# Optimization experiments

Measured on AMD Instinct MI355X. Metric: run time of the kernel, lower is better.

## Reference

```python
import jax, jax.numpy as jnp
import numpy as np

# (pt, eta, phi) feature indices per particle for each block (eta=None for MET)
A_PT, A_ETA, A_PHI = [5, 4, 35, 34], [9, 8, 45, 44], [13, 12, 55, 54]            # e3,e2,j9,j8
B_PT, B_ETA, B_PHI = [3, 33, 31, 2], [7, 43, 41, 6], [11, 53, 51, 10]            # e1,j7,j5,e0
C_PT, C_ETA, C_PHI = [28, 32, 15, 16], [38, 42, 19, 20], [48, 52, 23, 24]        # j2,j6,mu1,mu2
D_PT, D_ETA, D_PHI = [0, 14, 30, 26, 29, 27, 17], [None, 18, 40, 36, 39, 37, 21], [1, 22, 50, 46, 49, 47, 25]  # MET,mu0,j4,j0,j3,j1,mu3


def _bc(a, nd):
    # broadcast a (B,) or () angle factor over nd trailing qubit axes
    return a.reshape(a.shape + (1,) * nd)


def _rx(state, theta, w):
    nd = state.ndim - 2
    c = _bc(jnp.cos(theta * 0.5), nd)
    s = _bc(jnp.sin(theta * 0.5), nd)
    s0 = jnp.take(state, 0, axis=w + 1)
    s1 = jnp.take(state, 1, axis=w + 1)
    return jnp.stack([c * s0 - 1j * s * s1, -1j * s * s0 + c * s1], axis=w + 1)


def _ry(state, theta, w):
    nd = state.ndim - 2
    c = _bc(jnp.cos(theta * 0.5), nd)
    s = _bc(jnp.sin(theta * 0.5), nd)
    s0 = jnp.take(state, 0, axis=w + 1)
    s1 = jnp.take(state, 1, axis=w + 1)
    return jnp.stack([c * s0 - s * s1, s * s0 + c * s1], axis=w + 1)


def _rz(state, theta, w):
    nd = state.ndim - 2
    ph = _bc(jnp.exp(-0.5j * theta.astype(state.dtype)), nd)
    s0 = jnp.take(state, 0, axis=w + 1)
    s1 = jnp.take(state, 1, axis=w + 1)
    return jnp.stack([ph * s0, jnp.conj(ph) * s1], axis=w + 1)


def _cnot(state, ctrl, tgt):
    c0 = jnp.take(state, 0, axis=ctrl + 1)
    c1 = jnp.take(state, 1, axis=ctrl + 1)
    t_ax = tgt + 1 if tgt < ctrl else tgt  # ctrl axis removed shifts higher wires down
    c1 = jnp.flip(c1, axis=t_ax)
    return jnp.stack([c0, c1], axis=ctrl + 1)


def _extract(x, pt_idx, eta_idx, phi_idx):
    pt = x[:, np.array(pt_idx)]
    eta = jnp.stack([x[:, i] if i is not None else jnp.zeros(x.shape[0], x.dtype) for i in eta_idx], axis=1)
    phi = x[:, np.array(phi_idx)]
    return pt, eta, phi


def _run_block(pt, eta, phi, weights, n, latent, trash, depth):
    B = pt.shape[0]
    state = jnp.zeros((B,) + (2,) * n, dtype=jnp.complex64)
    state = state.at[(slice(None),) + (0,) * n].set(1.0)
    for k in range(n):
        state = _rx(state, eta[:, k], k)
        state = _ry(state, pt[:, k], k)
        state = _rz(state, phi[:, k], k)
    for k in range(n - 1):
        state = _cnot(state, k, k + 1)
    for k in range(n):
        state = _rz(state, eta[:, k], k)
        state = _ry(state, pt[:, k], k)
        state = _rx(state, phi[:, k], k)
    for d in range(depth):
        for t in trash:
            for l in latent:
                state = _cnot(state, t, l)
        for k in range(n):
            state = _ry(state, weights[d * n + k], k)
        for l in latent:
            for t in trash:
                state = _cnot(state, l, t)
    p = jnp.abs(state) ** 2  # (B, 2,...,2) real probabilities
    red = tuple(range(1, n))
    zs = [jnp.sum(jnp.take(p, 0, axis=w + 1), axis=red) - jnp.sum(jnp.take(p, 1, axis=w + 1), axis=red) for w in trash]
    return jnp.stack(zs, axis=1)


def setup_inputs() -> dict:
    key = jax.random.key(0)
    k0, k1, k2, k3, k4 = jax.random.split(key, 5)
    B = 131072
    x = jax.random.normal(k0, (B, 56), dtype=jnp.float32)
    wA = 0.01 * jax.random.normal(k1, (4,), dtype=jnp.float32)
    wB = 0.01 * jax.random.normal(k2, (4,), dtype=jnp.float32)
    wC = 0.01 * jax.random.normal(k3, (4,), dtype=jnp.float32)
    wD = 0.01 * jax.random.normal(k4, (28,), dtype=jnp.float32)
    return {"x": x, "wA": wA, "wB": wB, "wC": wC, "wD": wD}


def reference(x, wA, wB, wC, wD):
    zA = _run_block(*_extract(x, A_PT, A_ETA, A_PHI), wA, 4, (0, 1), (2, 3), 1)  # (B,2)
    zB = _run_block(*_extract(x, B_PT, B_ETA, B_PHI), wB, 4, (0, 1), (2, 3), 1)  # (B,2)
    zC = _run_block(*_extract(x, C_PT, C_ETA, C_PHI), wC, 4, (0, 1), (2, 3), 1)  # (B,2)
    zD = _run_block(*_extract(x, D_PT, D_ETA, D_PHI), wD, 7, (0, 1, 2, 3), (4, 5, 6), 4)  # (B,3)
    return jnp.concatenate([zA, zB, zC, zD], axis=1)  # (B,9) ~ dict values concatenated
```

## Files before the change

kernel.cpp:

```cpp
#include <hip/hip_runtime.h>
#include <hip/hip_fp16.h>


#define DEVINL __device__ __forceinline__

typedef _Float16 hv2 __attribute__((ext_vector_type(2)));

struct C2 { __half2 rr, mp; };

DEVINL C2 mkc(float re, float im) {
  C2 c; c.rr = __floats2half2_rn(re, re); c.mp = __floats2half2_rn(-im, im); return c;
}
DEVINL __half2 mkamp(float re, float im) { return __floats2half2_rn(re, im); }
DEVINL __half2 swap2(__half2 v) { return __lowhigh2highlow(v); }
DEVINL __half2 cmulc(C2 u, __half2 v) { return __hfma2(u.rr, v, __hmul2(u.mp, swap2(v))); }

DEVINL float ampsq(__half2 v, float acc) {
#if __has_builtin(__builtin_amdgcn_fdot2)
  return __builtin_amdgcn_fdot2(__builtin_bit_cast(hv2, v), __builtin_bit_cast(hv2, v), acc, false);
#else
  float2 f = __half22float2(v);
  return fmaf(f.x, f.x, fmaf(f.y, f.y, acc));
#endif
}

constexpr int parc(int x) { x ^= x >> 4; x ^= x >> 2; x ^= x >> 1; return x & 1; }

struct c32 { float x, y; };
DEVINL c32 cmulf(c32 a, c32 b) { return { a.x*b.x - a.y*b.y, a.x*b.y + a.y*b.x }; }


template<int N, int W>
DEVINL void g_ry(__half2* a, __half2 c2, __half2 s2, __half2 ns2) {
  constexpr int M = 1 << (N - 1 - W);
#pragma unroll
  for (int i = 0; i < (1 << N); ++i) if (!(i & M)) {
    const int j = i | M;
    __half2 v0 = a[i], v1 = a[j];
    a[i] = __hfma2(c2, v0, __hmul2(ns2, v1));
    a[j] = __hfma2(c2, v1, __hmul2(s2, v0));
  }
}

template<int N, int W>
DEVINL void g_u2(__half2* a, C2 u00, C2 u01, C2 u10, C2 u11) {
  constexpr int M = 1 << (N - 1 - W);
#pragma unroll
  for (int i = 0; i < (1 << N); ++i) if (!(i & M)) {
    const int j = i | M;
    __half2 v0 = a[i], v1 = a[j], v0s = swap2(v0), v1s = swap2(v1);
    a[i] = __hfma2(u00.rr, v0, __hfma2(u00.mp, v0s, __hfma2(u01.rr, v1, __hmul2(u01.mp, v1s))));
    a[j] = __hfma2(u10.rr, v0, __hfma2(u10.mp, v0s, __hfma2(u11.rr, v1, __hmul2(u11.mp, v1s))));
  }
}

template<int N, int C, int T>
DEVINL void g_cnot(__half2* a) {
  constexpr int CM = 1 << (N - 1 - C), TM = 1 << (N - 1 - T);
#pragma unroll
  for (int i = 0; i < (1 << N); ++i) if ((i & CM) && !(i & TM)) {
    const int j = i | TM;
    __half2 t = a[i]; a[i] = a[j]; a[j] = t;
  }
}

template<int N, int K>
DEVINL void chain_cnot(__half2* a) {
  if constexpr (K < N - 1) { g_cnot<N, K, K + 1>(a); chain_cnot<N, K + 1>(a); }
}


DEVINL void mk_u01(float ce, float se, float cp, float sp, float cf, float sf,
                   c32& u0, c32& u1) {
  u0 = cmulf({cf, -sf}, {cp * ce, sp * se});
  u1 = cmulf({cf,  sf}, {sp * ce, -cp * se});
}

DEVINL void mk_U(float ce, float se, float cp, float sp, float cf, float sf,
                 C2& U00, C2& U01, C2& U10, C2& U11) {
  c32 z = {ce, -se}, zb = {ce, se};
  c32 A = cmulf({cf * cp, -sf * sp}, z);
  c32 T = cmulf({cf * sp,  sf * cp}, zb);
  c32 Cc = cmulf({cf * sp, -sf * cp}, z);
  c32 D = cmulf({cf * cp,  sf * sp}, zb);
  U00 = mkc(A.x, A.y); U01 = mkc(-T.x, -T.y); U10 = mkc(Cc.x, Cc.y); U11 = mkc(D.x, D.y);
}

template<int N, int M>
DEVINL void build_step(__half2* a, const float* ce, const float* se, const float* cp,
                       const float* sp, const float* cf, const float* sf) {
  if constexpr (M < N) {
    c32 u0, u1; mk_u01(ce[M], se[M], cp[M], sp[M], cf[M], sf[M], u0, u1);
    C2 c0 = mkc(u0.x, u0.y), c1 = mkc(u1.x, u1.y);
#pragma unroll
    for (int j = (1 << M) - 1; j >= 0; --j) {
      __half2 s = a[j];
      a[2 * j]     = cmulc(c0, s);
      a[2 * j + 1] = cmulc(c1, s);
    }
    build_step<N, M + 1>(a, ce, se, cp, sp, cf, sf);
  }
}

template<int N, int K>
DEVINL void u_sweep(__half2* a, const float* ce, const float* se, const float* cp,
                    const float* sp, const float* cf, const float* sf) {
  if constexpr (K < N) {
    C2 U00, U01, U10, U11;
    mk_U(ce[K], se[K], cp[K], sp[K], cf[K], sf[K], U00, U01, U10, U11);
    g_u2<N, K>(a, U00, U01, U10, U11);
    u_sweep<N, K + 1>(a, ce, se, cp, sp, cf, sf);
  }
}

template<int N, int K>
DEVINL void ry_sweep(__half2* a, const __half2* c2, const __half2* s2, const __half2* ns2) {
  if constexpr (K < N) {
    g_ry<N, K>(a, c2[K], s2[K], ns2[K]);
    ry_sweep<N, K + 1>(a, c2, s2, ns2);
  }
}


template<int I>
DEVINL void sim4h(const float* r, const float* __restrict__ w, float* z) {
  constexpr int PT[3][4]  = {{5, 4, 35, 34}, {3, 33, 31, 2}, {28, 32, 15, 16}};
  constexpr int ETA[3][4] = {{9, 8, 45, 44}, {7, 43, 41, 6}, {38, 42, 19, 20}};
  constexpr int PHI[3][4] = {{13, 12, 55, 54}, {11, 53, 51, 10}, {48, 52, 23, 24}};
  float ce[4], se[4], cp[4], sp[4], cf[4], sf[4];
#pragma unroll
  for (int k = 0; k < 4; ++k) {
    __sincosf(0.5f * r[ETA[I][k]], &se[k], &ce[k]);
    __sincosf(0.5f * r[PT[I][k]],  &sp[k], &cp[k]);
    __sincosf(0.5f * r[PHI[I][k]], &sf[k], &cf[k]);
  }
  __half2 a[16];
  a[0] = mkamp(1.f, 0.f);
  build_step<4, 0>(a, ce, se, cp, sp, cf, sf);
  chain_cnot<4, 0>(a);
  u_sweep<4, 0>(a, ce, se, cp, sp, cf, sf);

#pragma unroll
  for (int i = 0; i < 16; ++i)
    if (parc(i & 3) && !(i & 8)) { __half2 t = a[i]; a[i] = a[i ^ 12]; a[i ^ 12] = t; }

  __half2 c2[4], s2[4], ns2[4];
#pragma unroll
  for (int k = 0; k < 4; ++k) {
    float sv, cv; __sincosf(0.5f * w[k], &sv, &cv);
    c2[k] = __floats2half2_rn(cv, cv);
    s2[k] = __floats2half2_rn(sv, sv);
    ns2[k] = __floats2half2_rn(-sv, -sv);
  }
  ry_sweep<4, 0>(a, c2, s2, ns2);

#pragma unroll
  for (int i = 0; i < 16; ++i)
    if (parc(i & 12) && !(i & 2)) { __half2 t = a[i]; a[i] = a[i ^ 3]; a[i ^ 3] = t; }

  float cls[4];
#pragma unroll
  for (int c = 0; c < 4; ++c) cls[c] = 0.f;
#pragma unroll
  for (int i = 0; i < 16; ++i) cls[i & 3] = ampsq(a[i], cls[i & 3]);
  float z0 = 0.f, z1 = 0.f;
#pragma unroll
  for (int c = 0; c < 4; ++c) {
    z0 += (c & 2) ? -cls[c] : cls[c];
    z1 += (c & 1) ? -cls[c] : cls[c];
  }
  z[0] = z0; z[1] = z1;
}


DEVINL void sim7h(const float* r, const float* __restrict__ wD, float* z) {
  constexpr int PT[7]  = {0, 14, 30, 26, 29, 27, 17};
  constexpr int ETA[7] = {-1, 18, 40, 36, 39, 37, 21};
  constexpr int PHI[7] = {1, 22, 50, 46, 49, 47, 25};
  float ce[7], se[7], cp[7], sp[7], cf[7], sf[7];
#pragma unroll
  for (int k = 0; k < 7; ++k) {
    float e = (ETA[k] < 0) ? 0.f : r[ETA[k]];
    __sincosf(0.5f * e, &se[k], &ce[k]);
    __sincosf(0.5f * r[PT[k]],  &sp[k], &cp[k]);
    __sincosf(0.5f * r[PHI[k]], &sf[k], &cf[k]);
  }
  __half2 a[128];
  a[0] = mkamp(1.f, 0.f);
  build_step<7, 0>(a, ce, se, cp, sp, cf, sf);
  chain_cnot<7, 0>(a);
  u_sweep<7, 0>(a, ce, se, cp, sp, cf, sf);

#pragma unroll 1
  for (int d = 0; d < 4; ++d) {
#pragma unroll
    for (int i = 0; i < 128; ++i)
      if (parc(i & 7) && !(i & 64)) { __half2 t = a[i]; a[i] = a[i ^ 0x78]; a[i ^ 0x78] = t; }

    __half2 c2[7], s2[7], ns2[7];
#pragma unroll
    for (int k = 0; k < 7; ++k) {
      float sv, cv; __sincosf(0.5f * wD[d * 7 + k], &sv, &cv);
      c2[k] = __floats2half2_rn(cv, cv);
      s2[k] = __floats2half2_rn(sv, sv);
      ns2[k] = __floats2half2_rn(-sv, -sv);
    }
    ry_sweep<7, 0>(a, c2, s2, ns2);

#pragma unroll
    for (int i = 0; i < 128; ++i)
      if (parc(i & 0x78) && !(i & 4)) { __half2 t = a[i]; a[i] = a[i ^ 7]; a[i ^ 7] = t; }
  }

  float cls[8];
#pragma unroll
  for (int c = 0; c < 8; ++c) cls[c] = 0.f;
#pragma unroll
  for (int i = 0; i < 128; ++i) cls[i & 7] = ampsq(a[i], cls[i & 7]);
  float z4 = 0.f, z5 = 0.f, z6 = 0.f;
#pragma unroll
  for (int c = 0; c < 8; ++c) {
    z4 += (c & 4) ? -cls[c] : cls[c];
    z5 += (c & 2) ? -cls[c] : cls[c];
    z6 += (c & 1) ? -cls[c] : cls[c];
  }
  z[0] = z4; z[1] = z5; z[2] = z6;
}


__global__ void __launch_bounds__(256, 2)
k_all(const float* __restrict__ x,
      const float* __restrict__ wA, const float* __restrict__ wB,
      const float* __restrict__ wC, const float* __restrict__ wD,
      float* __restrict__ out, int B) {
  const int b = blockIdx.x * blockDim.x + threadIdx.x;
  if (b >= B) return;

  float r[56];
  const float4* row4 = (const float4*)(x + (size_t)b * 56);
#pragma unroll
  for (int i = 0; i < 14; ++i) {
    float4 v = row4[i];
    r[4 * i] = v.x; r[4 * i + 1] = v.y; r[4 * i + 2] = v.z; r[4 * i + 3] = v.w;
  }

  float o[9];
  sim4h<0>(r, wA, &o[0]);
  sim4h<1>(r, wB, &o[2]);
  sim4h<2>(r, wC, &o[4]);
  sim7h(r, wD, &o[6]);

  float* op = out + (size_t)b * 9;
#pragma unroll
  for (int i = 0; i < 9; ++i) op[i] = o[i];
}


extern "C" void kernel_launch(void* const* d_in, const int* in_sizes, int n_in,
                              void* d_out, int out_size, void* d_ws, size_t ws_size,
                              hipStream_t stream) {
  const float* x  = (const float*)d_in[0];
  const float* wA = (const float*)d_in[1];
  const float* wB = (const float*)d_in[2];
  const float* wC = (const float*)d_in[3];
  const float* wD = (const float*)d_in[4];
  float* out = (float*)d_out;
  const int B = in_sizes[0] / 56;
  const int threads = 256;
  const int grid = (B + threads - 1) / threads;
  k_all<<<grid, threads, 0, stream>>>(x, wA, wB, wC, wD, out, B);
}
```

Measured before the change: 127.7 us.

## Split each event across two lanes with DPP exchange for the 7-qubit state

Each event is now handled by a pair of adjacent lanes. The lanes split blocks A and B between them, both compute block C redundantly, and the 7-qubit block D state is split by its top qubit into 64 amplitudes per lane. Gates on qubit 0 and the cross-half swaps use DPP lane exchanges, and the final Z sums are combined across the pair. The goal is to halve per-thread register pressure (128 to 64 half2 amplitudes) so occupancy can rise, with launch bounds raised to 3 blocks per SM. The cost is twice as many threads per event, redundant row loads and sincos work, and the duplicated block C computation.

```diff
diff --git a/kernel.cpp b/kernel.cpp
--- a/kernel.cpp
+++ b/kernel.cpp
@@ -24,6 +24,23 @@
 #endif
 }
 
+DEVINL __half2 dpph(__half2 v) {
+  int i = __builtin_bit_cast(int, v);
+  i = __builtin_amdgcn_mov_dpp(i, 0xB1, 0xF, 0xF, true);
+  return __builtin_bit_cast(__half2, i);
+}
+DEVINL float dppf(float v) {
+  int i = __builtin_bit_cast(int, v);
+  i = __builtin_amdgcn_mov_dpp(i, 0xB1, 0xF, 0xF, true);
+  return __builtin_bit_cast(float, i);
+}
+
+DEVINL __half2 selh(bool p, __half2 a, __half2 b) {
+  int ia = __builtin_bit_cast(int, a), ib = __builtin_bit_cast(int, b);
+  return __builtin_bit_cast(__half2, p ? ia : ib);
+}
+DEVINL float self_(bool p, float a, float b) { return p ? a : b; }
+
 constexpr int parc(int x) { x ^= x >> 4; x ^= x >> 2; x ^= x >> 1; return x & 1; }
 
 struct c32 { float x, y; };
@@ -64,11 +81,6 @@
   }
 }
 
-template<int N, int K>
-DEVINL void chain_cnot(__half2* a) {
-  if constexpr (K < N - 1) { g_cnot<N, K, K + 1>(a); chain_cnot<N, K + 1>(a); }
-}
-
 
 DEVINL void mk_u01(float ce, float se, float cp, float sp, float cf, float sf,
                    c32& u0, c32& u1) {
@@ -76,15 +88,23 @@
   u1 = cmulf({cf,  sf}, {sp * ce, -cp * se});
 }
 
+DEVINL void mk_Uf(float ce, float se, float cp, float sp, float cf, float sf,
+                  c32& A, c32& nT, c32& C, c32& D) {
+  c32 z = {ce, -se}, zb = {ce, se};
+  A = cmulf({cf * cp, -sf * sp}, z);
+  c32 T = cmulf({cf * sp,  sf * cp}, zb);
+  nT = {-T.x, -T.y};
+  C = cmulf({cf * sp, -sf * cp}, z);
+  D = cmulf({cf * cp,  sf * sp}, zb);
+}
+
 DEVINL void mk_U(float ce, float se, float cp, float sp, float cf, float sf,
                  C2& U00, C2& U01, C2& U10, C2& U11) {
-  c32 z = {ce, -se}, zb = {ce, se};
-  c32 A = cmulf({cf * cp, -sf * sp}, z);
-  c32 T = cmulf({cf * sp,  sf * cp}, zb);
-  c32 Cc = cmulf({cf * sp, -sf * cp}, z);
-  c32 D = cmulf({cf * cp,  sf * sp}, zb);
-  U00 = mkc(A.x, A.y); U01 = mkc(-T.x, -T.y); U10 = mkc(Cc.x, Cc.y); U11 = mkc(D.x, D.y);
-}
+  c32 A, nT, C, D;
+  mk_Uf(ce, se, cp, sp, cf, sf, A, nT, C, D);
+  U00 = mkc(A.x, A.y); U01 = mkc(nT.x, nT.y); U10 = mkc(C.x, C.y); U11 = mkc(D.x, D.y);
+}
+
 
 template<int N, int M>
 DEVINL void build_step(__half2* a, const float* ce, const float* se, const float* cp,
@@ -113,31 +133,19 @@
   }
 }
 
-template<int N, int K>
-DEVINL void ry_sweep(__half2* a, const __half2* c2, const __half2* s2, const __half2* ns2) {
-  if constexpr (K < N) {
-    g_ry<N, K>(a, c2[K], s2[K], ns2[K]);
-    ry_sweep<N, K + 1>(a, c2, s2, ns2);
-  }
-}
-
-
-template<int I>
-DEVINL void sim4h(const float* r, const float* __restrict__ w, float* z) {
-  constexpr int PT[3][4]  = {{5, 4, 35, 34}, {3, 33, 31, 2}, {28, 32, 15, 16}};
-  constexpr int ETA[3][4] = {{9, 8, 45, 44}, {7, 43, 41, 6}, {38, 42, 19, 20}};
-  constexpr int PHI[3][4] = {{13, 12, 55, 54}, {11, 53, 51, 10}, {48, 52, 23, 24}};
+DEVINL void sim4v(const float* eta, const float* pt, const float* phi,
+                  const float* wv, float* z) {
   float ce[4], se[4], cp[4], sp[4], cf[4], sf[4];
 #pragma unroll
   for (int k = 0; k < 4; ++k) {
-    __sincosf(0.5f * r[ETA[I][k]], &se[k], &ce[k]);
-    __sincosf(0.5f * r[PT[I][k]],  &sp[k], &cp[k]);
-    __sincosf(0.5f * r[PHI[I][k]], &sf[k], &cf[k]);
+    __sincosf(0.5f * eta[k], &se[k], &ce[k]);
+    __sincosf(0.5f * pt[k],  &sp[k], &cp[k]);
+    __sincosf(0.5f * phi[k], &sf[k], &cf[k]);
   }
   __half2 a[16];
   a[0] = mkamp(1.f, 0.f);
   build_step<4, 0>(a, ce, se, cp, sp, cf, sf);
-  chain_cnot<4, 0>(a);
+  g_cnot<4, 0, 1>(a); g_cnot<4, 1, 2>(a); g_cnot<4, 2, 3>(a);
   u_sweep<4, 0>(a, ce, se, cp, sp, cf, sf);
 
 #pragma unroll
@@ -147,20 +155,19 @@
   __half2 c2[4], s2[4], ns2[4];
 #pragma unroll
   for (int k = 0; k < 4; ++k) {
-    float sv, cv; __sincosf(0.5f * w[k], &sv, &cv);
+    float sv, cv; __sincosf(0.5f * wv[k], &sv, &cv);
     c2[k] = __floats2half2_rn(cv, cv);
     s2[k] = __floats2half2_rn(sv, sv);
     ns2[k] = __floats2half2_rn(-sv, -sv);
   }
-  ry_sweep<4, 0>(a, c2, s2, ns2);
+  g_ry<4, 0>(a, c2[0], s2[0], ns2[0]); g_ry<4, 1>(a, c2[1], s2[1], ns2[1]);
+  g_ry<4, 2>(a, c2[2], s2[2], ns2[2]); g_ry<4, 3>(a, c2[3], s2[3], ns2[3]);
 
 #pragma unroll
   for (int i = 0; i < 16; ++i)
     if (parc(i & 12) && !(i & 2)) { __half2 t = a[i]; a[i] = a[i ^ 3]; a[i ^ 3] = t; }
 
-  float cls[4];
-#pragma unroll
-  for (int c = 0; c < 4; ++c) cls[c] = 0.f;
+  float cls[4] = {0.f, 0.f, 0.f, 0.f};
 #pragma unroll
   for (int i = 0; i < 16; ++i) cls[i & 3] = ampsq(a[i], cls[i & 3]);
   float z0 = 0.f, z1 = 0.f;
@@ -173,7 +180,45 @@
 }
 
 
-DEVINL void sim7h(const float* r, const float* __restrict__ wD, float* z) {
+template<int K>
+DEVINL void d_build(__half2* a, const float* ce, const float* se, const float* cp,
+                    const float* sp, const float* cf, const float* sf) {
+  if constexpr (K <= 6) {
+    c32 u0, u1; mk_u01(ce[K], se[K], cp[K], sp[K], cf[K], sf[K], u0, u1);
+    C2 c0 = mkc(u0.x, u0.y), c1 = mkc(u1.x, u1.y);
+#pragma unroll
+    for (int j = (1 << (K - 1)) - 1; j >= 0; --j) {
+      __half2 s = a[j];
+      a[2 * j]     = cmulc(c0, s);
+      a[2 * j + 1] = cmulc(c1, s);
+    }
+    d_build<K + 1>(a, ce, se, cp, sp, cf, sf);
+  }
+}
+
+template<int K>
+DEVINL void d_usweep(__half2* a, const float* ce, const float* se, const float* cp,
+                     const float* sp, const float* cf, const float* sf) {
+  if constexpr (K <= 6) {
+    C2 U00, U01, U10, U11;
+    mk_U(ce[K], se[K], cp[K], sp[K], cf[K], sf[K], U00, U01, U10, U11);
+    g_u2<6, K - 1>(a, U00, U01, U10, U11);
+    d_usweep<K + 1>(a, ce, se, cp, sp, cf, sf);
+  }
+}
+
+template<int K>
+DEVINL void d_rysweep(__half2* a, const float* cw, const float* sw) {
+  if constexpr (K <= 6) {
+    __half2 c2 = __floats2half2_rn(cw[K], cw[K]);
+    __half2 s2 = __floats2half2_rn(sw[K], sw[K]);
+    __half2 ns2 = __floats2half2_rn(-sw[K], -sw[K]);
+    g_ry<6, K - 1>(a, c2, s2, ns2);
+    d_rysweep<K + 1>(a, cw, sw);
+  }
+}
+
+DEVINL void sim7_split(const float* r, const float* __restrict__ wD, bool p, float* z) {
   constexpr int PT[7]  = {0, 14, 30, 26, 29, 27, 17};
   constexpr int ETA[7] = {-1, 18, 40, 36, 39, 37, 21};
   constexpr int PHI[7] = {1, 22, 50, 46, 49, 47, 25};
@@ -185,38 +230,84 @@
     __sincosf(0.5f * r[PT[k]],  &sp[k], &cp[k]);
     __sincosf(0.5f * r[PHI[k]], &sf[k], &cf[k]);
   }
-  __half2 a[128];
-  a[0] = mkamp(1.f, 0.f);
-  build_step<7, 0>(a, ce, se, cp, sp, cf, sf);
-  chain_cnot<7, 0>(a);
-  u_sweep<7, 0>(a, ce, se, cp, sp, cf, sf);
-
-#pragma unroll 1
+
+  __half2 a[64];
+  {
+    c32 u0, u1; mk_u01(ce[0], se[0], cp[0], sp[0], cf[0], sf[0], u0, u1);
+    a[0] = mkamp(self_(p, u1.x, u0.x), self_(p, u1.y, u0.y));
+  }
+  d_build<1>(a, ce, se, cp, sp, cf, sf);
+
+#pragma unroll
+  for (int j = 0; j < 32; ++j) {
+    __half2 lo = a[j], hi = a[j + 32];
+    a[j] = selh(p, hi, lo);
+    a[j + 32] = selh(p, lo, hi);
+  }
+  g_cnot<6, 0, 1>(a); g_cnot<6, 1, 2>(a); g_cnot<6, 2, 3>(a);
+  g_cnot<6, 3, 4>(a); g_cnot<6, 4, 5>(a);
+
+  {
+    c32 A, nT, C, D;
+    mk_Uf(ce[0], se[0], cp[0], sp[0], cf[0], sf[0], A, nT, C, D);
+    C2 X = mkc(self_(p, D.x, A.x), self_(p, D.y, A.y));
+    C2 Y = mkc(self_(p, C.x, nT.x), self_(p, C.y, nT.y));
+#pragma unroll
+    for (int j = 0; j < 64; ++j) {
+      __half2 L = a[j], P = dpph(a[j]);
+      __half2 t = __hfma2(X.rr, L, __hmul2(X.mp, swap2(L)));
+      t = __hfma2(Y.rr, P, t);
+      a[j] = __hfma2(Y.mp, swap2(P), t);
+    }
+  }
+  d_usweep<1>(a, ce, se, cp, sp, cf, sf);
+
+#pragma unroll
   for (int d = 0; d < 4; ++d) {
 #pragma unroll
-    for (int i = 0; i < 128; ++i)
-      if (parc(i & 7) && !(i & 64)) { __half2 t = a[i]; a[i] = a[i ^ 0x78]; a[i ^ 0x78] = t; }
-
-    __half2 c2[7], s2[7], ns2[7];
-#pragma unroll
-    for (int k = 0; k < 7; ++k) {
-      float sv, cv; __sincosf(0.5f * wD[d * 7 + k], &sv, &cv);
-      c2[k] = __floats2half2_rn(cv, cv);
-      s2[k] = __floats2half2_rn(sv, sv);
-      ns2[k] = __floats2half2_rn(-sv, -sv);
-    }
-    ry_sweep<7, 0>(a, c2, s2, ns2);
-
-#pragma unroll
-    for (int i = 0; i < 128; ++i)
-      if (parc(i & 0x78) && !(i & 4)) { __half2 t = a[i]; a[i] = a[i ^ 7]; a[i ^ 7] = t; }
-  }
-
-  float cls[8];
-#pragma unroll
-  for (int c = 0; c < 8; ++c) cls[c] = 0.f;
-#pragma unroll
-  for (int i = 0; i < 128; ++i) cls[i & 7] = ampsq(a[i], cls[i & 7]);
+    for (int j = 0; j < 64; ++j) {
+      if (parc(j & 7) && !(j & 0x20)) {
+        const int k = j ^ 0x38;
+        __half2 t1 = dpph(a[j]), t2 = dpph(a[k]);
+        a[j] = t2; a[k] = t1;
+      }
+    }
+
+    float cw[7], sw[7];
+#pragma unroll
+    for (int k = 0; k < 7; ++k) __sincosf(0.5f * wD[d * 7 + k], &sw[k], &cw[k]);
+
+    {
+      __half2 c2 = __floats2half2_rn(cw[0], cw[0]);
+      float bb = self_(p, sw[0], -sw[0]);
+      __half2 b2 = __floats2half2_rn(bb, bb);
+#pragma unroll
+      for (int j = 0; j < 64; ++j) {
+        __half2 P = dpph(a[j]);
+        a[j] = __hfma2(c2, a[j], __hmul2(b2, P));
+      }
+    }
+    d_rysweep<1>(a, cw, sw);
+
+#pragma unroll
+    for (int j = 0; j < 64; ++j) {
+      if (!(j & 4)) {
+        const int k = j ^ 7;
+        __half2 lo = a[j], hi = a[k];
+        if (parc(j & 0x38)) {
+          a[j] = selh(p, lo, hi);
+          a[k] = selh(p, hi, lo);
+        } else {
+          a[j] = selh(p, hi, lo);
+          a[k] = selh(p, lo, hi);
+        }
+      }
+    }
+  }
+
+  float cls[8] = {0.f, 0.f, 0.f, 0.f, 0.f, 0.f, 0.f, 0.f};
+#pragma unroll
+  for (int j = 0; j < 64; ++j) cls[j & 7] = ampsq(a[j], cls[j & 7]);
   float z4 = 0.f, z5 = 0.f, z6 = 0.f;
 #pragma unroll
   for (int c = 0; c < 8; ++c) {
@@ -224,35 +315,65 @@
     z5 += (c & 2) ? -cls[c] : cls[c];
     z6 += (c & 1) ? -cls[c] : cls[c];
   }
-  z[0] = z4; z[1] = z5; z[2] = z6;
-}
-
-
-__global__ void __launch_bounds__(256, 2)
+  z[0] = z4 + dppf(z4);
+  z[1] = z5 + dppf(z5);
+  z[2] = z6 + dppf(z6);
+}
+
+
+__global__ void __launch_bounds__(256, 3)
 k_all(const float* __restrict__ x,
       const float* __restrict__ wA, const float* __restrict__ wB,
       const float* __restrict__ wC, const float* __restrict__ wD,
       float* __restrict__ out, int B) {
-  const int b = blockIdx.x * blockDim.x + threadIdx.x;
-  if (b >= B) return;
+  const int tid = threadIdx.x;
+  const bool p = (tid & 1);
+  const int e = blockIdx.x * 128 + (tid >> 1);
+  if (e >= B) return;
 
   float r[56];
-  const float4* row4 = (const float4*)(x + (size_t)b * 56);
+  const float4* row4 = (const float4*)(x + (size_t)e * 56);
 #pragma unroll
   for (int i = 0; i < 14; ++i) {
     float4 v = row4[i];
     r[4 * i] = v.x; r[4 * i + 1] = v.y; r[4 * i + 2] = v.z; r[4 * i + 3] = v.w;
   }
-
-  float o[9];
-  sim4h<0>(r, wA, &o[0]);
-  sim4h<1>(r, wB, &o[2]);
-  sim4h<2>(r, wC, &o[4]);
-  sim7h(r, wD, &o[6]);
-
-  float* op = out + (size_t)b * 9;
-#pragma unroll
-  for (int i = 0; i < 9; ++i) op[i] = o[i];
+  float* op = out + (size_t)e * 9;
+
+  {
+    constexpr int PTA[4] = {5, 4, 35, 34}, ETAA[4] = {9, 8, 45, 44}, PHIA[4] = {13, 12, 55, 54};
+    constexpr int PTB[4] = {3, 33, 31, 2}, ETAB[4] = {7, 43, 41, 6}, PHIB[4] = {11, 53, 51, 10};
+    float pe[4], pp[4], pf[4], wv[4];
+#pragma unroll
+    for (int k = 0; k < 4; ++k) {
+      pe[k] = self_(p, r[ETAB[k]], r[ETAA[k]]);
+      pp[k] = self_(p, r[PTB[k]],  r[PTA[k]]);
+      pf[k] = self_(p, r[PHIB[k]], r[PHIA[k]]);
+      wv[k] = self_(p, wB[k], wA[k]);
+    }
+    float z2[2];
+    sim4v(pe, pp, pf, wv, z2);
+    const int base = p ? 2 : 0;
+    op[base] = z2[0]; op[base + 1] = z2[1];
+  }
+
+  {
+    constexpr int PTC[4] = {28, 32, 15, 16}, ETAC[4] = {38, 42, 19, 20}, PHIC[4] = {48, 52, 23, 24};
+    float pe[4], pp[4], pf[4], wv[4];
+#pragma unroll
+    for (int k = 0; k < 4; ++k) {
+      pe[k] = r[ETAC[k]]; pp[k] = r[PTC[k]]; pf[k] = r[PHIC[k]]; wv[k] = wC[k];
+    }
+    float z2[2];
+    sim4v(pe, pp, pf, wv, z2);
+    if (!p) { op[4] = z2[0]; op[5] = z2[1]; }
+  }
+
+  {
+    float z3[3];
+    sim7_split(r, wD, p, z3);
+    if (p) { op[6] = z3[0]; op[7] = z3[1]; op[8] = z3[2]; }
+  }
 }
 
 
@@ -266,7 +387,6 @@
   const float* wD = (const float*)d_in[4];
   float* out = (float*)d_out;
   const int B = in_sizes[0] / 56;
-  const int threads = 256;
-  const int grid = (B + threads - 1) / threads;
-  k_all<<<grid, threads, 0, stream>>>(x, wA, wB, wC, wD, out, B);
-}
+  const int grid = (B + 127) / 128;
+  k_all<<<grid, 256, 0, stream>>>(x, wA, wB, wC, wD, out, B);
+}
```

Result: slower. 153.1 us (+19.9%).
